# Performance work log

Hardware: AMD Instinct MI355X
Metric: run time of the kernel (lower is better)

## Reference

```python
import jax, jax.numpy as jnp
import numpy as np


def setup_inputs() -> dict:
    key = jax.random.key(0)
    k1, k2 = jax.random.split(key)
    B, C, H, W = 4, 64, 256, 512
    right_input = jax.random.normal(k1, (B, C, H, W), dtype=jnp.float32)
    disparity_samples = jax.random.uniform(k2, (B, 1, H, W), dtype=jnp.float32)
    return {"right_input": right_input, "disparity_samples": disparity_samples}


def reference(right_input, disparity_samples):
    B, C, H, W = right_input.shape
    dt = right_input.dtype
    # left pixel x-coordinates along width, broadcast over B,1,H
    left_y = jnp.arange(W, dtype=dt).reshape(1, 1, 1, W)
    right_y = left_y + disparity_samples                      # [B,1,H,W]
    ry_a = jnp.floor(right_y)
    ry_b = ry_a + 1.0
    wa = ry_b - right_y                                       # [B,1,H,W]
    wb = right_y - ry_a
    idx_a = jnp.clip(ry_a, 0, W - 1).astype(jnp.int32)
    idx_b = jnp.clip(ry_b, 0, W - 1).astype(jnp.int32)
    # broadcast indices across channels and gather along width (dim=3)
    idx_a = jnp.broadcast_to(idx_a, (B, C, H, W))
    idx_b = jnp.broadcast_to(idx_b, (B, C, H, W))
    feat_a = jnp.take_along_axis(right_input, idx_a, axis=3)
    feat_b = jnp.take_along_axis(right_input, idx_b, axis=3)
    warped = wa * feat_a + wb * feat_b                        # weights broadcast over C
    # zero out samples whose (unclamped) coordinate fell outside [0, W-1]
    oob = (right_y < 0).astype(dt) + (right_y > (W - 1)).astype(dt)
    return (1.0 - oob) * warped
```

## Files before the change

kernel.cpp:

```cpp
#include <hip/hip_runtime.h>

constexpr int B = 4;
constexpr int C = 64;
constexpr int H = 256;
constexpr int W = 512;
constexpr int CH_PER_BLOCK = 16;
constexpr int ROWS_PER_ITER = 2;

__global__ __launch_bounds__(256) void spatial_warp_kernel(
    const float* __restrict__ input,
    const float* __restrict__ disp,
    float* __restrict__ out)
{
    __shared__ float s_row[ROWS_PER_ITER * W];
    __shared__ float s_disp[W];

    const int t = threadIdx.x;
    const int cg = blockIdx.x % (C / CH_PER_BLOCK);
    int rest = blockIdx.x / (C / CH_PER_BLOCK);
    const int h = rest % H;
    const int b = rest / H;
    const int c_base = cg * CH_PER_BLOCK;

    const long long pix_base = ((long long)b * H + h) * W;
    if (t < W / 4) {
        reinterpret_cast<float4*>(s_disp)[t] =
            reinterpret_cast<const float4*>(disp + pix_base)[t];
    }
    __syncthreads();

    const int r     = t >> 7;
    const int lane7 = t & 127;

    float wa4[4], wb4[4], msk[4];
    int   ia4[4], ib4[4];
#pragma unroll
    for (int i = 0; i < 4; ++i) {
        const int w  = lane7 + 128 * i;
        const float d  = s_disp[w];
        const float ry = (float)w + d;
        const float ra = floorf(ry);
        const float rb = ra + 1.0f;
        wa4[i] = rb - ry;
        wb4[i] = ry - ra;
        ia4[i] = (int)fminf(fmaxf(ra, 0.0f), (float)(W - 1));
        ib4[i] = (int)fminf(fmaxf(rb, 0.0f), (float)(W - 1));
        msk[i] = (ry >= 0.0f && ry <= (float)(W - 1)) ? 1.0f : 0.0f;
    }

    const int lds_base = r * W;
#pragma unroll 2
    for (int cc = 0; cc < CH_PER_BLOCK / ROWS_PER_ITER; ++cc) {
        const int c_mine = c_base + cc * ROWS_PER_ITER + r;
        const float* rowg = input + (((long long)b * C + c_mine) * H + h) * (long long)W;
        const float4 v = reinterpret_cast<const float4*>(rowg)[lane7];
        __syncthreads();
        reinterpret_cast<float4*>(s_row + lds_base)[lane7] = v;
        __syncthreads();

        float* outg = out + (((long long)b * C + c_mine) * H + h) * (long long)W;
#pragma unroll
        for (int i = 0; i < 4; ++i) {
            const int w = lane7 + 128 * i;
            const float fa = s_row[lds_base + ia4[i]];
            const float fb = s_row[lds_base + ib4[i]];
            outg[w] = msk[i] * (wa4[i] * fa + wb4[i] * fb);
        }
    }
}

extern "C" void kernel_launch(void* const* d_in, const int* in_sizes, int n_in,
                              void* d_out, int out_size, void* d_ws, size_t ws_size,
                              hipStream_t stream) {
    const float* input = (const float*)d_in[0];
    const float* disp  = (const float*)d_in[1];
    float* outp = (float*)d_out;

    const int grid = B * H * (C / CH_PER_BLOCK);
    spatial_warp_kernel<<<grid, 256, 0, stream>>>(input, disp, outp);
}
```

Before: 234.5 us.

## Stage rows per wave in padded LDS with prefetch and vector stores

Each wave now owns its own double-buffered LDS row slice and processes 4 channels. This removes every block-wide __syncthreads. The disparity row is read straight from global memory as float4, and the OOB mask is folded into the interpolation weights. The next channel's row is prefetched into registers, LDS rows are padded to reduce bank conflicts on the gathers, and outputs are written as float4. The risk is unaligned 16-byte LDS writes caused by the padding, plus reliance on wave-level execution ordering instead of explicit barriers.

New measurement: 238.0 us. Within noise of the previous version (+1.5%).

```diff
diff --git a/kernel.cpp b/kernel.cpp
--- a/kernel.cpp
+++ b/kernel.cpp
@@ -4,68 +4,89 @@
 constexpr int C = 64;
 constexpr int H = 256;
 constexpr int W = 512;
-constexpr int CH_PER_BLOCK = 16;
-constexpr int ROWS_PER_ITER = 2;
+constexpr int CPB = 16;
+constexpr int CPW = 4;
+constexpr int WPAD = W + W / 32;
 
-__global__ __launch_bounds__(256) void spatial_warp_kernel(
+__global__ __launch_bounds__(256, 8) void spatial_warp_kernel(
     const float* __restrict__ input,
     const float* __restrict__ disp,
     float* __restrict__ out)
 {
-    __shared__ float s_row[ROWS_PER_ITER * W];
-    __shared__ float s_disp[W];
+    __shared__ float s_row[4][2][WPAD];
 
-    const int t = threadIdx.x;
-    const int cg = blockIdx.x % (C / CH_PER_BLOCK);
-    int rest = blockIdx.x / (C / CH_PER_BLOCK);
-    const int h = rest % H;
-    const int b = rest / H;
-    const int c_base = cg * CH_PER_BLOCK;
+    const int t    = threadIdx.x;
+    const int wave = t >> 6;
+    const int lane = t & 63;
 
-    const long long pix_base = ((long long)b * H + h) * W;
-    if (t < W / 4) {
-        reinterpret_cast<float4*>(s_disp)[t] =
-            reinterpret_cast<const float4*>(disp + pix_base)[t];
-    }
-    __syncthreads();
+    const int cg = blockIdx.x & 3;
+    const int h  = (blockIdx.x >> 2) & (H - 1);
+    const int b  = blockIdx.x >> 10;
 
-    const int r     = t >> 7;
-    const int lane7 = t & 127;
+    const int p0 = lane * 4;
+    const int p1 = 256 + p0;
 
-    float wa4[4], wb4[4], msk[4];
-    int   ia4[4], ib4[4];
+    const long long pixb = ((long long)b * H + h) * (long long)W;
+    const float4 d0 = *reinterpret_cast<const float4*>(disp + pixb + p0);
+    const float4 d1 = *reinterpret_cast<const float4*>(disp + pixb + p1);
+    const float dv[8] = {d0.x, d0.y, d0.z, d0.w, d1.x, d1.y, d1.z, d1.w};
+
+    float wa[8], wb[8];
+    int   jj[8];
 #pragma unroll
-    for (int i = 0; i < 4; ++i) {
-        const int w  = lane7 + 128 * i;
-        const float d  = s_disp[w];
-        const float ry = (float)w + d;
+    for (int j = 0; j < 8; ++j) {
+        const int w   = (j < 4) ? (p0 + j) : (p1 + j - 4);
+        const float ry = (float)w + dv[j];
         const float ra = floorf(ry);
-        const float rb = ra + 1.0f;
-        wa4[i] = rb - ry;
-        wb4[i] = ry - ra;
-        ia4[i] = (int)fminf(fmaxf(ra, 0.0f), (float)(W - 1));
-        ib4[i] = (int)fminf(fmaxf(rb, 0.0f), (float)(W - 1));
-        msk[i] = (ry >= 0.0f && ry <= (float)(W - 1)) ? 1.0f : 0.0f;
+        const float m  = (ry >= 0.0f && ry <= (float)(W - 1)) ? 1.0f : 0.0f;
+        wa[j] = m * ((ra + 1.0f) - ry);
+        wb[j] = m * (ry - ra);
+        const int ia = (int)fminf(fmaxf(ra, 0.0f), (float)(W - 1));
+        const int ib = min(ia + 1, W - 1);
+        const int iap = ia + (ia >> 5);
+        const int ibp = ib + (ib >> 5);
+        jj[j] = iap | (ibp << 16);
     }
 
-    const int lds_base = r * W;
-#pragma unroll 2
-    for (int cc = 0; cc < CH_PER_BLOCK / ROWS_PER_ITER; ++cc) {
-        const int c_mine = c_base + cc * ROWS_PER_ITER + r;
-        const float* rowg = input + (((long long)b * C + c_mine) * H + h) * (long long)W;
-        const float4 v = reinterpret_cast<const float4*>(rowg)[lane7];
-        __syncthreads();
-        reinterpret_cast<float4*>(s_row + lds_base)[lane7] = v;
-        __syncthreads();
+    const int c0 = cg * CPB + wave * CPW;
+    const long long base    = (((long long)b * C + c0) * H + h) * (long long)W;
+    const long long cstride = (long long)H * W;
+    const float* __restrict__ gin  = input + base;
+    float*       __restrict__ gout = out + base;
 
-        float* outg = out + (((long long)b * C + c_mine) * H + h) * (long long)W;
+    const int wp0 = p0 + (p0 >> 5);
+    const int wp1 = p1 + (p1 >> 5);
+
+    float4 va = *reinterpret_cast<const float4*>(gin + p0);
+    float4 vb = *reinterpret_cast<const float4*>(gin + p1);
+
 #pragma unroll
-        for (int i = 0; i < 4; ++i) {
-            const int w = lane7 + 128 * i;
-            const float fa = s_row[lds_base + ia4[i]];
-            const float fb = s_row[lds_base + ib4[i]];
-            outg[w] = msk[i] * (wa4[i] * fa + wb4[i] * fb);
+    for (int cc = 0; cc < CPW; ++cc) {
+        float4 na, nb;
+        if (cc + 1 < CPW) {
+            na = *reinterpret_cast<const float4*>(gin + (cc + 1) * cstride + p0);
+            nb = *reinterpret_cast<const float4*>(gin + (cc + 1) * cstride + p1);
         }
+
+        float* sb = s_row[wave][cc & 1];
+        *reinterpret_cast<float4*>(sb + wp0) = va;
+        *reinterpret_cast<float4*>(sb + wp1) = vb;
+
+        float ov[8];
+#pragma unroll
+        for (int j = 0; j < 8; ++j) {
+            const int iap = jj[j] & 0xFFFF;
+            const int ibp = jj[j] >> 16;
+            ov[j] = wa[j] * sb[iap] + wb[j] * sb[ibp];
+        }
+
+        float4 o0 = {ov[0], ov[1], ov[2], ov[3]};
+        float4 o1 = {ov[4], ov[5], ov[6], ov[7]};
+        *reinterpret_cast<float4*>(gout + cc * cstride + p0) = o0;
+        *reinterpret_cast<float4*>(gout + cc * cstride + p1) = o1;
+
+        va = na;
+        vb = nb;
     }
 }
 
@@ -76,6 +97,6 @@
     const float* disp  = (const float*)d_in[1];
     float* outp = (float*)d_out;
 
-    const int grid = B * H * (C / CH_PER_BLOCK);
+    const int grid = B * H * (C / CPB);
     spatial_warp_kernel<<<grid, 256, 0, stream>>>(input, disp, outp);
 }
```
